# Performance work log

Hardware: AMD Instinct MI355X
Metric: run time of the kernel (lower is better)

## Reference

```python
import jax, jax.numpy as jnp
import numpy as np

B, S, D_IN, H, D_HEAD = 8, 1024, 768, 12, 64

def setup_inputs() -> dict:
    key = jax.random.key(0)
    k1, k2, k3, k4 = jax.random.split(key, 4)
    x = jax.random.normal(k1, (B, S, D_IN), dtype=jnp.float32)
    # per-head projection weights, stacked: [H, d_in, d_head]
    scale = 1.0 / np.sqrt(D_IN)
    Wq = jax.random.normal(k2, (H, D_IN, D_HEAD), dtype=jnp.float32) * scale
    Wk = jax.random.normal(k3, (H, D_IN, D_HEAD), dtype=jnp.float32) * scale
    Wv = jax.random.normal(k4, (H, D_IN, D_HEAD), dtype=jnp.float32) * scale
    return {"x": x, "Wq": Wq, "Wk": Wk, "Wv": Wv}

def reference(x, Wq, Wk, Wv) -> jnp.ndarray:
    # Batched equivalent of the Python loop over heads + concat.
    q = jnp.einsum('bsd,hde->bhse', x, Wq)  # [B,H,S,Dh]
    k = jnp.einsum('bsd,hde->bhse', x, Wk)
    v = jnp.einsum('bsd,hde->bhse', x, Wv)
    scores = jnp.einsum('bhse,bhte->bhst', q, k) / jnp.sqrt(jnp.asarray(D_HEAD, x.dtype))
    causal = jnp.tril(jnp.ones((S, S), dtype=bool))  # [S,S]
    scores = jnp.where(causal, scores, jnp.asarray(-jnp.inf, x.dtype))
    attn = jax.nn.softmax(scores, axis=-1)  # dropout p=0.0 -> identity
    ctx = jnp.einsum('bhst,bhte->bhse', attn, v)  # [B,H,S,Dh]
    # concat heads along last dim -> [B,S,H*Dh]
    return jnp.transpose(ctx, (0, 2, 1, 3)).reshape(B, S, H * D_HEAD)
```

## Files before the change

kernel.cpp:

```cpp
#include <hip/hip_runtime.h>

typedef short short8 __attribute__((ext_vector_type(8)));
typedef float f32x4 __attribute__((ext_vector_type(4)));
typedef float f32x16 __attribute__((ext_vector_type(16)));

#define SQ   1024
#define DIN  768
#define NH   12
#define DH   64
#define SCL2 0.1803368801111243f

static __device__ __forceinline__ ushort f2bf(float f) {
  union { float f; unsigned u; } v; v.f = f;
  unsigned u = v.u;
  unsigned r = (u + 0x7FFFu + ((u >> 16) & 1u)) >> 16;
  return (ushort)r;
}
static __device__ __forceinline__ unsigned pk2(float a, float b) {
  return (unsigned)f2bf(a) | ((unsigned)f2bf(b) << 16);
}

static __device__ __forceinline__ void gload_lds16(const ushort* g, ushort* l) {
  __builtin_amdgcn_global_load_lds(
      (const __attribute__((address_space(1))) unsigned*)(g),
      (__attribute__((address_space(3))) unsigned*)(l),
      16, 0, 0);
}

__global__ __launch_bounds__(256) void k_convert_x(const float* __restrict__ x,
                                                   ushort* __restrict__ xb) {
  int i = (blockIdx.x * 256 + threadIdx.x) * 4;
  float4 v = *reinterpret_cast<const float4*>(x + i);
  ushort4 o;
  o.x = f2bf(v.x); o.y = f2bf(v.y); o.z = f2bf(v.z); o.w = f2bf(v.w);
  *reinterpret_cast<ushort4*>(xb + i) = o;
}

__global__ __launch_bounds__(256) void k_prep_w(const float* __restrict__ Wq,
                                                const float* __restrict__ Wk,
                                                const float* __restrict__ Wv,
                                                ushort* __restrict__ wt) {
  __shared__ ushort tile[64][65];
  const int mh = blockIdx.x;
  const int m = mh / 12, h = mh % 12;
  const int d0 = blockIdx.y * 64;
  const float* W = (m == 0 ? Wq : (m == 1 ? Wk : Wv)) + h * DIN * DH;
  ushort* outp = wt + (size_t)mh * DH * DIN;
  #pragma unroll
  for (int p = 0; p < 16; ++p) {
    int idx = p * 256 + threadIdx.x;
    int d = idx >> 6, e = idx & 63;
    tile[d][e] = f2bf(W[(d0 + d) * DH + e]);
  }
  __syncthreads();
  #pragma unroll
  for (int p = 0; p < 16; ++p) {
    int idx = p * 256 + threadIdx.x;
    int e = idx >> 6, d = idx & 63;
    outp[e * DIN + d0 + d] = tile[d][e];
  }
}

__global__ __launch_bounds__(256) void k_proj(const ushort* __restrict__ xb,
                                              const ushort* __restrict__ wt,
                                              ushort* __restrict__ qo,
                                              ushort* __restrict__ ko,
                                              ushort* __restrict__ vto) {
  __shared__ __align__(16) ushort Ab[3][128][32];
  __shared__ __align__(16) ushort Bb[3][128][32];

  const int brow = blockIdx.x * 128;
  const int bn   = blockIdx.y * 128;
  const int w    = threadIdx.x >> 6, lane = threadIdx.x & 63;
  const int lr   = lane & 15, lg = lane >> 4;
  const int wm   = w >> 1, wn = w & 1;

  const int srow  = threadIdx.x >> 2;
  const int sslot = (threadIdx.x & 3) ^ (srow & 3) ^ ((srow >> 2) & 3);
  const ushort* gA = xb + (size_t)(brow + srow) * DIN + sslot * 8;
  const ushort* gB = wt + (size_t)(bn   + srow) * DIN + sslot * 8;

  f32x4 acc[4][4];
  #pragma unroll
  for (int i = 0; i < 4; ++i)
    #pragma unroll
    for (int j = 0; j < 4; ++j) acc[i][j] = (f32x4){0.f, 0.f, 0.f, 0.f};

  const int fr   = (lr & 3) ^ ((lr >> 2) & 3);
  const int aoff = (lg ^ fr) * 8;

#define STAGE(bi, tt) do {                                                \
    const int k0_ = (tt) * 32;                                            \
    ushort* la_ = &Ab[bi][0][0] + threadIdx.x * 8;                        \
    ushort* lb_ = &Bb[bi][0][0] + threadIdx.x * 8;                        \
    gload_lds16(gA + k0_,            la_);                                \
    gload_lds16(gA + k0_ + 64 * DIN, la_ + 2048);                         \
    gload_lds16(gB + k0_,            lb_);                                \
    gload_lds16(gB + k0_ + 64 * DIN, lb_ + 2048);                         \
  } while (0)

  STAGE(0, 0);
  STAGE(1, 1);

  int cur = 0;
  #pragma unroll 1
  for (int t = 0; t < 24; ++t) {
    if (t < 23) {
      asm volatile("s_waitcnt vmcnt(4)" ::: "memory");
    } else {
      asm volatile("s_waitcnt vmcnt(0)" ::: "memory");
    }
    __builtin_amdgcn_sched_barrier(0);
    __builtin_amdgcn_s_barrier();
    __builtin_amdgcn_sched_barrier(0);
    if (t + 2 < 24) {
      int nb = cur + 2; if (nb >= 3) nb -= 3;
      STAGE(nb, t + 2);
    }
    short8 a[4], b[4];
    #pragma unroll
    for (int mi = 0; mi < 4; ++mi)
      a[mi] = *reinterpret_cast<const short8*>(&Ab[cur][wm * 64 + mi * 16 + lr][aoff]);
    #pragma unroll
    for (int ci = 0; ci < 4; ++ci)
      b[ci] = *reinterpret_cast<const short8*>(&Bb[cur][wn * 64 + ci * 16 + lr][aoff]);
    #pragma unroll
    for (int mi = 0; mi < 4; ++mi)
      #pragma unroll
      for (int ci = 0; ci < 4; ++ci)
        acc[mi][ci] = __builtin_amdgcn_mfma_f32_16x16x32_bf16(a[mi], b[ci], acc[mi][ci], 0, 0, 0);
    cur += 1; if (cur >= 3) cur = 0;
  }
#undef STAGE

  const int mh = (bn + wn * 64) >> 6;
  const int m = mh / 12, h = mh % 12;
  const int lgq = lane >> 4;
  #pragma unroll
  for (int mi = 0; mi < 4; ++mi)
    #pragma unroll
    for (int ci = 0; ci < 4; ++ci)
      #pragma unroll
      for (int r = 0; r < 4; ++r) {
        int rg = brow + wm * 64 + mi * 16 + lgq * 4 + r;
        int b_ = rg >> 10, sl = rg & 1023;
        int bh = b_ * 12 + h;
        int e  = ci * 16 + lr;
        ushort val = f2bf(acc[mi][ci][r]);
        if (m == 2) {
          vto[((size_t)bh * DH + e) * SQ + sl] = val;
        } else {
          ushort* dst = (m == 0) ? qo : ko;
          dst[((size_t)bh * SQ + sl) * DH + e] = val;
        }
      }
}

__global__ __launch_bounds__(256, 3) void k_attn(const ushort* __restrict__ qi,
                                                 const ushort* __restrict__ ki,
                                                 const ushort* __restrict__ vti,
                                                 float* __restrict__ out) {
  __shared__ __align__(16) ushort Kb[2][64 * 64];
  __shared__ __align__(16) ushort Vb[2][64 * 64];

  const int f = blockIdx.x;
  const int g = f >> 8, r_ = f & 255;
  const int qt = ((r_ & 7) + g * 3) & 7;
  const int bh = g * 32 + (r_ >> 3);
  const int b = bh / 12, h = bh % 12;
  const int w = threadIdx.x >> 6, lane = threadIdx.x & 63;
  const int ql = lane & 31, hi = lane >> 5;
  const int q0 = qt * 128 + w * 32;
  const int nt = (q0 >> 6) + 1;
  const int ntmax = 2 * qt + 2;
  const ushort* qb = qi  + (size_t)bh * SQ * DH;
  const ushort* kb = ki  + (size_t)bh * SQ * DH;
  const ushort* vb = vti + (size_t)bh * DH * SQ;

  short8 qf[4];
  #pragma unroll
  for (int m = 0; m < 4; ++m)
    qf[m] = *reinterpret_cast<const short8*>(qb + (size_t)(q0 + ql) * DH + m * 16 + hi * 8);

  f32x16 o0, o1;
  #pragma unroll
  for (int r = 0; r < 16; ++r) { o0[r] = 0.f; o1[r] = 0.f; }
  float m_run = -1e30f, l_run = 0.f;

#define STAGE(bufi, tt) do {                                                                   \
    const int kv0_ = (tt) * 64;                                                                \
    const int t0 = threadIdx.x, t1 = threadIdx.x + 256;                                        \
    gload_lds16(kb + (size_t)(kv0_ + (t0 >> 3)) * DH + (((t0 & 7) ^ ((t0 >> 3) & 7)) * 8),     \
                &Kb[bufi][0] + t0 * 8);                                                        \
    gload_lds16(kb + (size_t)(kv0_ + (t1 >> 3)) * DH + (((t1 & 7) ^ ((t1 >> 3) & 7)) * 8),     \
                &Kb[bufi][0] + t1 * 8);                                                        \
    gload_lds16(vb + (size_t)(t0 >> 3) * SQ + kv0_ + (((t0 & 7) ^ ((t0 >> 3) & 7)) * 8),       \
                &Vb[bufi][0] + t0 * 8);                                                        \
    gload_lds16(vb + (size_t)(t1 >> 3) * SQ + kv0_ + (((t1 & 7) ^ ((t1 >> 3) & 7)) * 8),       \
                &Vb[bufi][0] + t1 * 8);                                                        \
  } while (0)

  STAGE(0, 0);
  __syncthreads();

  int cur = 0;
  #pragma unroll 1
  for (int t = 0; t < ntmax; ++t) {
    if (t + 1 < ntmax) STAGE(cur ^ 1, t + 1);

    if (t < nt) {
      const int kv0 = t * 64;
      const ushort* Kc = &Kb[cur][0];
      const ushort* Vc = &Vb[cur][0];

      f32x16 s0, s1;
      #pragma unroll
      for (int r = 0; r < 16; ++r) { s0[r] = 0.f; s1[r] = 0.f; }
      #pragma unroll
      for (int m = 0; m < 4; ++m) {
        short8 kf = *reinterpret_cast<const short8*>(Kc + ql * 64 + ((2 * m + hi) ^ (ql & 7)) * 8);
        s0 = __builtin_amdgcn_mfma_f32_32x32x16_bf16(kf, qf[m], s0, 0, 0, 0);
      }
      #pragma unroll
      for (int m = 0; m < 4; ++m) {
        short8 kf = *reinterpret_cast<const short8*>(Kc + (32 + ql) * 64 + ((2 * m + hi) ^ (ql & 7)) * 8);
        s1 = __builtin_amdgcn_mfma_f32_32x32x16_bf16(kf, qf[m], s1, 0, 0, 0);
      }

      if (t == nt - 1) {
        const int qg = q0 + ql;
        #pragma unroll
        for (int r = 0; r < 16; ++r) {
          int kvl = (r & 3) + 8 * (r >> 2) + 4 * hi;
          if (kv0 + kvl      > qg) s0[r] = -1e30f;
          if (kv0 + 32 + kvl > qg) s1[r] = -1e30f;
        }
      }

      float mt = s0[0];
      #pragma unroll
      for (int r = 1; r < 16; ++r) mt = fmaxf(mt, s0[r]);
      #pragma unroll
      for (int r = 0; r < 16; ++r) mt = fmaxf(mt, s1[r]);
      mt = fmaxf(mt, __shfl_xor(mt, 32));
      if (__any(mt > m_run + 40.0f)) {
        float mnew = fmaxf(m_run, mt);
        float corr = exp2f((m_run - mnew) * SCL2);
        l_run *= corr; m_run = mnew;
        #pragma unroll
        for (int r = 0; r < 16; ++r) {
          float cr = __shfl(corr, (r & 3) + 8 * (r >> 2) + 4 * hi);
          o0[r] *= cr; o1[r] *= cr;
        }
      }
      float ts = 0.f;
      #pragma unroll
      for (int r = 0; r < 16; ++r) {
        s0[r] = exp2f((s0[r] - m_run) * SCL2); ts += s0[r];
        s1[r] = exp2f((s1[r] - m_run) * SCL2); ts += s1[r];
      }
      ts += __shfl_xor(ts, 32);
      l_run += ts;

#define PV_CHUNK(SV, CC, KC) do {                                                              \
        unsigned wa = pk2(SV[(CC) * 8 + 0], SV[(CC) * 8 + 1]);                                 \
        unsigned wb = pk2(SV[(CC) * 8 + 2], SV[(CC) * 8 + 3]);                                 \
        unsigned wc = pk2(SV[(CC) * 8 + 4], SV[(CC) * 8 + 5]);                                 \
        unsigned wd = pk2(SV[(CC) * 8 + 6], SV[(CC) * 8 + 7]);                                 \
        unsigned xa = __shfl_xor(wa, 32), xb2 = __shfl_xor(wb, 32);                            \
        unsigned xc = __shfl_xor(wc, 32), xd = __shfl_xor(wd, 32);                             \
        uint4 pw;                                                                              \
        pw.x = hi ? xc : wa;  pw.y = hi ? xd : wb;                                             \
        pw.z = hi ? wc : xa;  pw.w = hi ? wd : xb2;                                            \
        short8 pa = *reinterpret_cast<short8*>(&pw);                                           \
        short8 vf0 = *reinterpret_cast<const short8*>(Vc + ql * 64 +                           \
                       ((2 * (KC) + hi) ^ (ql & 7)) * 8);                                      \
        o0 = __builtin_amdgcn_mfma_f32_32x32x16_bf16(pa, vf0, o0, 0, 0, 0);                    \
        short8 vf1 = *reinterpret_cast<const short8*>(Vc + (32 + ql) * 64 +                    \
                       ((2 * (KC) + hi) ^ (ql & 7)) * 8);                                      \
        o1 = __builtin_amdgcn_mfma_f32_32x32x16_bf16(pa, vf1, o1, 0, 0, 0);                    \
      } while (0)

      PV_CHUNK(s0, 0, 0);
      PV_CHUNK(s0, 1, 1);
      PV_CHUNK(s1, 0, 2);
      PV_CHUNK(s1, 1, 3);
#undef PV_CHUNK
    }

    __syncthreads();
    cur ^= 1;
  }
#undef STAGE

  float rl = 1.0f / l_run;
  #pragma unroll
  for (int r = 0; r < 16; ++r) {
    int base = (r & 3) + 8 * (r >> 2) + 4 * hi;
    float sc_ = __shfl(rl, base);
    int qg = q0 + base;
    float* op = out + ((size_t)b * SQ + qg) * (NH * DH) + h * DH;
    op[ql]      = o0[r] * sc_;
    op[32 + ql] = o1[r] * sc_;
  }
}

extern "C" void kernel_launch(void* const* d_in, const int* in_sizes, int n_in,
                              void* d_out, int out_size, void* d_ws, size_t ws_size,
                              hipStream_t stream) {
  const float* x  = (const float*)d_in[0];
  const float* Wq = (const float*)d_in[1];
  const float* Wk = (const float*)d_in[2];
  const float* Wv = (const float*)d_in[3];
  float* out = (float*)d_out;

  char* ws = (char*)d_ws;
  ushort* xb = (ushort*)(ws);
  ushort* wt = (ushort*)(ws + 12582912);
  ushort* q  = (ushort*)(ws + 16121856);
  ushort* k  = (ushort*)(ws + 28704768);
  ushort* vt = (ushort*)(ws + 41287680);

  k_convert_x<<<6144, 256, 0, stream>>>(x, xb);
  k_prep_w<<<dim3(36, 12), 256, 0, stream>>>(Wq, Wk, Wv, wt);
  k_proj<<<dim3(64, 18), 256, 0, stream>>>(xb, wt, q, k, vt);
  k_attn<<<768, 256, 0, stream>>>(q, k, vt, out);
}
```

Baseline: 199.8 us.

## Stage projection epilogue through LDS for vectorized stores; switch to double buffering

```diff
diff --git a/kernel.cpp b/kernel.cpp
--- a/kernel.cpp
+++ b/kernel.cpp
@@ -66,8 +66,7 @@
                                               ushort* __restrict__ qo,
                                               ushort* __restrict__ ko,
                                               ushort* __restrict__ vto) {
-  __shared__ __align__(16) ushort Ab[3][128][32];
-  __shared__ __align__(16) ushort Bb[3][128][32];
+  __shared__ __align__(16) ushort Sb[16384];
 
   const int brow = blockIdx.x * 128;
   const int bn   = blockIdx.y * 128;
@@ -89,71 +88,88 @@
   const int fr   = (lr & 3) ^ ((lr >> 2) & 3);
   const int aoff = (lg ^ fr) * 8;
 
-#define STAGE(bi, tt) do {                                                \
+#define STAGEP(bi, tt) do {                                               \
     const int k0_ = (tt) * 32;                                            \
-    ushort* la_ = &Ab[bi][0][0] + threadIdx.x * 8;                        \
-    ushort* lb_ = &Bb[bi][0][0] + threadIdx.x * 8;                        \
+    ushort* la_ = Sb + (bi) * 4096 + threadIdx.x * 8;                     \
+    ushort* lb_ = Sb + 8192 + (bi) * 4096 + threadIdx.x * 8;              \
     gload_lds16(gA + k0_,            la_);                                \
     gload_lds16(gA + k0_ + 64 * DIN, la_ + 2048);                         \
     gload_lds16(gB + k0_,            lb_);                                \
     gload_lds16(gB + k0_ + 64 * DIN, lb_ + 2048);                         \
   } while (0)
 
-  STAGE(0, 0);
-  STAGE(1, 1);
+  STAGEP(0, 0);
+  __syncthreads();
 
   int cur = 0;
   #pragma unroll 1
   for (int t = 0; t < 24; ++t) {
-    if (t < 23) {
-      asm volatile("s_waitcnt vmcnt(4)" ::: "memory");
-    } else {
-      asm volatile("s_waitcnt vmcnt(0)" ::: "memory");
-    }
-    __builtin_amdgcn_sched_barrier(0);
-    __builtin_amdgcn_s_barrier();
-    __builtin_amdgcn_sched_barrier(0);
-    if (t + 2 < 24) {
-      int nb = cur + 2; if (nb >= 3) nb -= 3;
-      STAGE(nb, t + 2);
-    }
+    if (t + 1 < 24) STAGEP(cur ^ 1, t + 1);
     short8 a[4], b[4];
     #pragma unroll
     for (int mi = 0; mi < 4; ++mi)
-      a[mi] = *reinterpret_cast<const short8*>(&Ab[cur][wm * 64 + mi * 16 + lr][aoff]);
+      a[mi] = *reinterpret_cast<const short8*>(&Sb[cur * 4096 + (wm * 64 + mi * 16 + lr) * 32 + aoff]);
     #pragma unroll
     for (int ci = 0; ci < 4; ++ci)
-      b[ci] = *reinterpret_cast<const short8*>(&Bb[cur][wn * 64 + ci * 16 + lr][aoff]);
+      b[ci] = *reinterpret_cast<const short8*>(&Sb[8192 + cur * 4096 + (wn * 64 + ci * 16 + lr) * 32 + aoff]);
     #pragma unroll
     for (int mi = 0; mi < 4; ++mi)
       #pragma unroll
       for (int ci = 0; ci < 4; ++ci)
         acc[mi][ci] = __builtin_amdgcn_mfma_f32_16x16x32_bf16(a[mi], b[ci], acc[mi][ci], 0, 0, 0);
-    cur += 1; if (cur >= 3) cur = 0;
-  }
-#undef STAGE
-
-  const int mh = (bn + wn * 64) >> 6;
+    __syncthreads();
+    cur ^= 1;
+  }
+#undef STAGEP
+
+  ushort* ldsw = Sb + w * 4096;
+  const int colbase = bn + wn * 64;
+  const int mh = colbase >> 6;
   const int m = mh / 12, h = mh % 12;
-  const int lgq = lane >> 4;
-  #pragma unroll
-  for (int mi = 0; mi < 4; ++mi)
-    #pragma unroll
-    for (int ci = 0; ci < 4; ++ci)
-      #pragma unroll
-      for (int r = 0; r < 4; ++r) {
-        int rg = brow + wm * 64 + mi * 16 + lgq * 4 + r;
-        int b_ = rg >> 10, sl = rg & 1023;
-        int bh = b_ * 12 + h;
-        int e  = ci * 16 + lr;
-        ushort val = f2bf(acc[mi][ci][r]);
-        if (m == 2) {
-          vto[((size_t)bh * DH + e) * SQ + sl] = val;
-        } else {
-          ushort* dst = (m == 0) ? qo : ko;
-          dst[((size_t)bh * SQ + sl) * DH + e] = val;
+  const int c = lane & 7;
+
+  if (m < 2) {
+    #pragma unroll
+    for (int mi = 0; mi < 4; ++mi)
+      #pragma unroll
+      for (int ci = 0; ci < 4; ++ci)
+        #pragma unroll
+        for (int r = 0; r < 4; ++r) {
+          int sl = mi * 16 + lg * 4 + r;
+          int e  = ci * 16 + lr;
+          ldsw[sl * 64 + (e ^ ((sl & 7) << 3))] = f2bf(acc[mi][ci][r]);
         }
-      }
+    asm volatile("s_waitcnt lgkmcnt(0)" ::: "memory");
+    ushort* dst = (m == 0) ? qo : ko;
+    #pragma unroll
+    for (int it = 0; it < 8; ++it) {
+      int sl = it * 8 + (lane >> 3);
+      short8 vv = *reinterpret_cast<const short8*>(&ldsw[sl * 64 + ((c * 8) ^ ((sl & 7) << 3))]);
+      int rg = brow + wm * 64 + sl;
+      int b_ = rg >> 10, s_ = rg & 1023;
+      *reinterpret_cast<short8*>(dst + ((size_t)(b_ * 12 + h) * SQ + s_) * DH + c * 8) = vv;
+    }
+  } else {
+    #pragma unroll
+    for (int mi = 0; mi < 4; ++mi)
+      #pragma unroll
+      for (int ci = 0; ci < 4; ++ci)
+        #pragma unroll
+        for (int r = 0; r < 4; ++r) {
+          int sl = mi * 16 + lg * 4 + r;
+          int e  = ci * 16 + lr;
+          ldsw[e * 64 + (sl ^ ((e & 7) << 3))] = f2bf(acc[mi][ci][r]);
+        }
+    asm volatile("s_waitcnt lgkmcnt(0)" ::: "memory");
+    #pragma unroll
+    for (int it = 0; it < 8; ++it) {
+      int e = it * 8 + (lane >> 3);
+      short8 vv = *reinterpret_cast<const short8*>(&ldsw[e * 64 + ((c * 8) ^ ((e & 7) << 3))]);
+      int rg = brow + wm * 64 + c * 8;
+      int b_ = rg >> 10, s_ = rg & 1023;
+      *reinterpret_cast<short8*>(vto + ((size_t)(b_ * 12 + h) * DH + e) * SQ + s_) = vv;
+    }
+  }
 }
 
 __global__ __launch_bounds__(256, 3) void k_attn(const ushort* __restrict__ qi,
```

Result: faster. 177.7 us (-11.1%).
